# Optimization experiments

Measured on AMD Instinct MI355X. Metric: run time of the kernel, lower is better.

## Reference

```python
import jax, jax.numpy as jnp
import numpy as np

D_MODEL = 1024
N_HEADS = 16
D_K = D_MODEL // N_HEADS
B, S = 8, 1024
EPS = 1e-8


def setup_inputs() -> dict:
    key = jax.random.key(0)
    ks = jax.random.split(key, 6)
    scale = 1.0 / np.sqrt(D_MODEL)
    return {
        "Q_in": jax.random.normal(ks[0], (B, S, D_MODEL), jnp.float32),
        "mask": jax.random.randint(ks[1], (B, 1, S, S), 0, 2, jnp.int32),
        "Wq": jax.random.normal(ks[2], (D_MODEL, D_MODEL), jnp.float32) * scale,
        "bq": jnp.zeros((D_MODEL,), jnp.float32),
        "Wk": jax.random.normal(ks[3], (D_MODEL, D_MODEL), jnp.float32) * scale,
        "bk": jnp.zeros((D_MODEL,), jnp.float32),
        "Wv": jax.random.normal(ks[4], (D_MODEL, D_MODEL), jnp.float32) * scale,
        "bv": jnp.zeros((D_MODEL,), jnp.float32),
        "Wo": jax.random.normal(ks[5], (D_MODEL, D_MODEL), jnp.float32) * scale,
        "bo": jnp.zeros((D_MODEL,), jnp.float32),
    }


def reference(Q_in, mask, Wq, bq, Wk, bk, Wv, bv, Wo, bo):
    # QKV projections: [B,S,D] -> [B,H,S,d_k]
    def split_heads(x):
        return x.reshape(B, S, N_HEADS, D_K).transpose(0, 2, 1, 3)

    Q = split_heads(Q_in @ Wq + bq)
    K = split_heads(Q_in @ Wk + bk)
    V = split_heads(Q_in @ Wv + bv)

    # scaled scores [B,H,S,S], standard softmax
    scores = jnp.einsum("bhqd,bhkd->bhqk", Q, K) / jnp.sqrt(
        jnp.asarray(D_K, jnp.float32))
    scores = jax.nn.softmax(scores, axis=-1)
    # non-standard: multiplicative mask AFTER softmax, then row renorm
    scores = scores * mask.astype(scores.dtype)
    attn = scores / (jnp.sum(scores, axis=-1, keepdims=True) + EPS)

    context = jnp.einsum("bhqk,bhkd->bhqd", attn, V)
    context = context.transpose(0, 2, 1, 3).reshape(B, S, D_MODEL)
    return context @ Wo + bo
```

## Files before the change

### kernel.cpp

```cpp
#include <hip/hip_runtime.h>
#include <hip/hip_bf16.h>
#include <stdint.h>

typedef __attribute__((ext_vector_type(4))) float f32x4;
typedef __attribute__((ext_vector_type(8))) __bf16 bf16x8;
typedef unsigned short u16;
typedef unsigned int u32;
typedef unsigned long long u64;

#define NH 16
#define DKK 64

__device__ __forceinline__ u16 f2bf(float f) {
    u32 u = __builtin_bit_cast(u32, f);
    u32 r = (u + 0x7fffu + ((u >> 16) & 1u)) >> 16;
    return (u16)r;
}

__device__ __forceinline__ u16 cvt_bf(float f) {
    __hip_bfloat16 h = __float2bfloat16(f);
    return *reinterpret_cast<u16*>(&h);
}

__device__ __forceinline__ void gload16(const void* g, void* l) {
    __builtin_amdgcn_global_load_lds((const __attribute__((address_space(1))) void*)g,
                                     (__attribute__((address_space(3))) void*)l, 16, 0, 0);
}

__global__ __launch_bounds__(256) void k_convert_x(const float* __restrict__ x,
                                                   u16* __restrict__ xb) {
    int i = blockIdx.x * 256 + threadIdx.x;
    const float4* p = (const float4*)x + (size_t)i * 2;
    float4 a = p[0], b = p[1];
    union { u16 h[8]; uint4 q; } o;
    o.h[0] = f2bf(a.x); o.h[1] = f2bf(a.y); o.h[2] = f2bf(a.z); o.h[3] = f2bf(a.w);
    o.h[4] = f2bf(b.x); o.h[5] = f2bf(b.y); o.h[6] = f2bf(b.z); o.h[7] = f2bf(b.w);
    ((uint4*)xb)[i] = o.q;
}

__global__ __launch_bounds__(256) void k_convert_w(const float* __restrict__ wq,
                                                   const float* __restrict__ wk,
                                                   const float* __restrict__ wv,
                                                   const float* __restrict__ wo,
                                                   u16* __restrict__ wt) {
    int z = blockIdx.z;
    const float* w = (z == 0) ? wq : (z == 1) ? wk : (z == 2) ? wv : wo;
    __shared__ float t[32][33];
    int tx = threadIdx.x & 31, ty = threadIdx.x >> 5;
    int n0 = blockIdx.x * 32, k0 = blockIdx.y * 32;
    for (int rr = 0; rr < 4; ++rr)
        t[ty + rr * 8][tx] = w[(size_t)(k0 + ty + rr * 8) * 1024 + n0 + tx];
    __syncthreads();
    for (int rr = 0; rr < 4; ++rr) {
        int n = n0 + ty + rr * 8;
        wt[((size_t)z * 1024 + n) * 1024 + k0 + tx] = f2bf(t[tx][ty + rr * 8]);
    }
}

__global__ __launch_bounds__(256) void k_maskpack(const int* __restrict__ mask,
                                                  u64* __restrict__ mb) {
    int wid = (blockIdx.x * 256 + threadIdx.x) >> 6;
    int lane = threadIdx.x & 63;
    for (int c = wid; c < 8 * 1024 * 16; c += 8192) {
        int m = mask[(size_t)c * 64 + lane];
        u64 bits = __ballot(m != 0);
        if (lane == 0)
            mb[(c & 0xFFFFC000u) | ((c & 15) << 10) | ((c >> 4) & 1023)] = bits;
    }
}

template <int MODE>
__global__ __launch_bounds__(256) void k_gemm(const u16* __restrict__ A,
                                              const u16* __restrict__ Bt,
                                              const float* __restrict__ b0,
                                              const float* __restrict__ b1,
                                              const float* __restrict__ b2,
                                              u16* __restrict__ q_out,
                                              u16* __restrict__ k_out,
                                              u16* __restrict__ v_out,
                                              float* __restrict__ out) {
    __shared__ u16 As[128 * 32];
    __shared__ u16 Bs[128 * 32];
    int tid = threadIdx.x;
    int wv = tid >> 6, lane = tid & 63;
    int r = lane & 15, g = lane >> 4;
    int wr = wv >> 1, wc = wv & 1;
    int m0 = blockIdx.x * 128, n0 = blockIdx.y * 128;
    f32x4 acc[4][4] = {};
    for (int kt = 0; kt < 1024; kt += 32) {
        __syncthreads();
        for (int i = 0; i < 2; ++i) {
            int e = i * 256 + tid;
            int row = e >> 2, c8 = (e & 3) * 8;
            const u16* ga = A + (size_t)(m0 + row) * 1024 + kt + c8;
            const u16* gb = Bt + (size_t)(n0 + row) * 1024 + kt + c8;
            gload16(ga, As + (size_t)(i * 256 + wv * 64) * 8);
            gload16(gb, Bs + (size_t)(i * 256 + wv * 64) * 8);
        }
        __syncthreads();
        bf16x8 aF[4], bF[4];
        for (int m = 0; m < 4; ++m) aF[m] = *(const bf16x8*)&As[(wr * 64 + m * 16 + r) * 32 + g * 8];
        for (int n = 0; n < 4; ++n) bF[n] = *(const bf16x8*)&Bs[(wc * 64 + n * 16 + r) * 32 + g * 8];
        for (int m = 0; m < 4; ++m)
            for (int n = 0; n < 4; ++n)
                acc[m][n] = __builtin_amdgcn_mfma_f32_16x16x32_bf16(aF[m], bF[n], acc[m][n], 0, 0, 0);
    }
    for (int m = 0; m < 4; ++m) {
        int rowb = m0 + wr * 64 + m * 16 + 4 * g;
        for (int n = 0; n < 4; ++n) {
            int col = n0 + wc * 64 + n * 16 + r;
            if (MODE == 0) {
                int w = col >> 10, cn = col & 1023;
                const float* bp = (w == 0) ? b0 : (w == 1) ? b1 : b2;
                u16* dst = (w == 0) ? q_out : (w == 1) ? k_out : v_out;
                float sc = (w == 0) ? 0.125f : 1.0f;
                int h = cn >> 6, d = cn & 63;
                float bias = bp[cn];
                for (int i = 0; i < 4; ++i) {
                    int row = rowb + i;
                    int b = row >> 10, s = row & 1023;
                    float v = (acc[m][n][i] + bias) * sc;
                    dst[((size_t)(b * NH + h) * 1024 + s) * 64 + d] = f2bf(v);
                }
            } else {
                float bias = b0[col];
                for (int i = 0; i < 4; ++i) {
                    int row = rowb + i;
                    out[(size_t)row * 1024 + col] = acc[m][n][i] + bias;
                }
            }
        }
    }
}

__global__ __launch_bounds__(256) void k_transpose_v(const u16* __restrict__ vb,
                                                     u16* __restrict__ vt) {
    __shared__ u16 t[64][72];
    int bh = blockIdx.y, s0 = blockIdx.x * 64;
    int tid = threadIdx.x;
    for (int i = 0; i < 2; ++i) {
        int e = i * 256 + tid;
        int row = e >> 3, ch = (e & 7) * 8;
        uint4 v = *(const uint4*)(vb + ((size_t)bh * 1024 + s0 + row) * 64 + ch);
        *(uint4*)&t[row][ch] = v;
    }
    __syncthreads();
    for (int i = 0; i < 2; ++i) {
        int e = i * 256 + tid;
        int d = e >> 3, ch = (e & 7) * 8;
        union { u16 h[8]; uint4 q; } o;
        for (int j = 0; j < 8; ++j) o.h[j] = t[ch + j][d];
        *(uint4*)(vt + ((size_t)bh * 64 + d) * 1024 + s0 + ch) = o.q;
    }
}

__global__ __launch_bounds__(256, 3) void k_attn(const u16* __restrict__ qb,
                                                 const u16* __restrict__ kb,
                                                 const u16* __restrict__ vt,
                                                 const u64* __restrict__ mbits,
                                                 u16* __restrict__ ctx) {
    __shared__ u16 Kd[2][64 * 64];
    __shared__ u16 Vd[2][64 * 64];
    int tid = threadIdx.x, wv = tid >> 6, lane = tid & 63;
    int r = lane & 15, g = lane >> 4;
    int q0 = blockIdx.x * 128, bh = blockIdx.y;
    int b = bh >> 4, h = bh & 15;

    bf16x8 aq[2][2];
    for (int qg = 0; qg < 2; ++qg) {
        const u16* qp = qb + ((size_t)bh * 1024 + q0 + wv * 32 + qg * 16 + r) * 64 + g * 8;
        aq[qg][0] = *(const bf16x8*)qp;
        aq[qg][1] = *(const bf16x8*)(qp + 32);
    }

    f32x4 of[2][4] = {};
    f32x4 zacc[2] = {};
    const bf16x8 vone = {(__bf16)1.f, (__bf16)1.f, (__bf16)1.f, (__bf16)1.f,
                         (__bf16)1.f, (__bf16)1.f, (__bf16)1.f, (__bf16)1.f};

    const u64* mrow = mbits + ((size_t)b * 16) * 1024 + q0 + wv * 32 + r;
    u64 mbc[2] = {mrow[0], mrow[16]};

    for (int i2 = 0; i2 < 2; ++i2) {
        int e = i2 * 256 + tid;
        int s = e >> 3, c = e & 7;
        int cs = (c ^ (s & 7)) * 8;
        int kr = (s & 0x20) | ((s & 0x0C) << 1) | ((s & 0x10) >> 2) | (s & 3);
        gload16(kb + ((size_t)bh * 1024 + kr) * 64 + cs, Kd[0] + (size_t)e * 8);
        gload16(vt + ((size_t)bh * 64 + s) * 1024 + cs, Vd[0] + (size_t)e * 8);
    }
    __syncthreads();

    for (int t = 0; t < 16; ++t) {
        int cur = t & 1;
        u64 mbn0 = 0, mbn1 = 0;
        if (t < 15) {
            int ktn = (t + 1) * 64;
            for (int i2 = 0; i2 < 2; ++i2) {
                int e = i2 * 256 + tid;
                int s = e >> 3, c = e & 7;
                int cs = (c ^ (s & 7)) * 8;
                int kr = (s & 0x20) | ((s & 0x0C) << 1) | ((s & 0x10) >> 2) | (s & 3);
                gload16(kb + ((size_t)bh * 1024 + ktn + kr) * 64 + cs, Kd[cur ^ 1] + (size_t)e * 8);
                gload16(vt + ((size_t)bh * 64 + s) * 1024 + ktn + cs, Vd[cur ^ 1] + (size_t)e * 8);
            }
            mbn0 = mrow[(size_t)(t + 1) * 1024];
            mbn1 = mrow[(size_t)(t + 1) * 1024 + 16];
        }
        const u16* K = Kd[cur];
        const u16* V = Vd[cur];

        bf16x8 bk0[4], bk1[4];
#pragma unroll
        for (int nf = 0; nf < 4; ++nf) {
            int rowk = (nf * 16 + r) * 64;
            bk0[nf] = *(const bf16x8*)&K[rowk + ((g ^ (r & 7)) << 3)];
            bk1[nf] = *(const bf16x8*)&K[rowk + (((g + 4) ^ (r & 7)) << 3)];
        }

        bf16x8 pfr[2][2];
#pragma unroll
        for (int qg = 0; qg < 2; ++qg) {
            f32x4 sf[4];
#pragma unroll
            for (int nf = 0; nf < 4; ++nf) {
                f32x4 z = {0.f, 0.f, 0.f, 0.f};
                z = __builtin_amdgcn_mfma_f32_16x16x32_bf16(bk0[nf], aq[qg][0], z, 0, 0, 0);
                sf[nf] = __builtin_amdgcn_mfma_f32_16x16x32_bf16(bk1[nf], aq[qg][1], z, 0, 0, 0);
            }
            u64 m64 = mbc[qg] >> (g * 8);
            u32 mlo = (u32)m64, mhi = (u32)(m64 >> 32);
            u32 pw[8];
#pragma unroll
            for (int nf = 0; nf < 4; ++nf) {
                u32 nib = ((nf & 2) ? mhi : mlo) >> ((nf & 1) * 4);
                u32 pm0 = ((nib & 1) ? 0xFFFFu : 0u) | ((nib & 2) ? 0xFFFF0000u : 0u);
                u32 pm1 = ((nib & 4) ? 0xFFFFu : 0u) | ((nib & 8) ? 0xFFFF0000u : 0u);
                float e0 = __expf(sf[nf][0]), e1 = __expf(sf[nf][1]);
                float e2 = __expf(sf[nf][2]), e3 = __expf(sf[nf][3]);
                pw[2 * nf]     = (((u32)cvt_bf(e0)) | ((u32)cvt_bf(e1) << 16)) & pm0;
                pw[2 * nf + 1] = (((u32)cvt_bf(e2)) | ((u32)cvt_bf(e3) << 16)) & pm1;
            }
            union { u32 w[4]; bf16x8 v; } f0, f1;
            f0.w[0] = pw[0]; f0.w[1] = pw[1]; f0.w[2] = pw[2]; f0.w[3] = pw[3];
            f1.w[0] = pw[4]; f1.w[1] = pw[5]; f1.w[2] = pw[6]; f1.w[3] = pw[7];
            pfr[qg][0] = f0.v;
            pfr[qg][1] = f1.v;
            zacc[qg] = __builtin_amdgcn_mfma_f32_16x16x32_bf16(vone, pfr[qg][0], zacc[qg], 0, 0, 0);
            zacc[qg] = __builtin_amdgcn_mfma_f32_16x16x32_bf16(vone, pfr[qg][1], zacc[qg], 0, 0, 0);
        }
#pragma unroll
        for (int ks = 0; ks < 2; ++ks) {
#pragma unroll
            for (int nf = 0; nf < 4; ++nf) {
                bf16x8 av = *(const bf16x8*)&V[(nf * 16 + r) * 64 + (((ks * 4 + g) ^ (r & 7)) << 3)];
                of[0][nf] = __builtin_amdgcn_mfma_f32_16x16x32_bf16(av, pfr[0][ks], of[0][nf], 0, 0, 0);
                of[1][nf] = __builtin_amdgcn_mfma_f32_16x16x32_bf16(av, pfr[1][ks], of[1][nf], 0, 0, 0);
            }
        }
        mbc[0] = mbn0;
        mbc[1] = mbn1;
        __syncthreads();
    }

    for (int qg = 0; qg < 2; ++qg) {
        float inv = 1.0f / zacc[qg][0];
        int qrow = q0 + wv * 32 + qg * 16 + r;
        u16* crow = ctx + ((size_t)(b * 1024 + qrow)) * 1024 + h * 64;
#pragma unroll
        for (int nf = 0; nf < 4; ++nf) {
            u32 w0 = ((u32)cvt_bf(of[qg][nf][0] * inv)) | ((u32)cvt_bf(of[qg][nf][1] * inv) << 16);
            u32 w1 = ((u32)cvt_bf(of[qg][nf][2] * inv)) | ((u32)cvt_bf(of[qg][nf][3] * inv) << 16);
            *(u32*)(crow + nf * 16 + g * 4) = w0;
            *(u32*)(crow + nf * 16 + g * 4 + 2) = w1;
        }
    }
}

extern "C" void kernel_launch(void* const* d_in, const int* in_sizes, int n_in,
                              void* d_out, int out_size, void* d_ws, size_t ws_size,
                              hipStream_t stream) {
    const float* Q_in = (const float*)d_in[0];
    const int*   mask = (const int*)d_in[1];
    const float* Wq = (const float*)d_in[2];
    const float* bq = (const float*)d_in[3];
    const float* Wk = (const float*)d_in[4];
    const float* bk = (const float*)d_in[5];
    const float* Wv = (const float*)d_in[6];
    const float* bv = (const float*)d_in[7];
    const float* Wo = (const float*)d_in[8];
    const float* bo = (const float*)d_in[9];

    char* ws = (char*)d_ws;
    u16* Xb = (u16*)(ws);
    u16* Wt = (u16*)(ws + 16777216);
    u16* Qb = (u16*)(ws + 25165824);
    u16* Kb = (u16*)(ws + 41943040);
    u16* Vb = (u16*)(ws + 58720256);
    u16* Vt = (u16*)(ws + 75497472);
    u64* Mb = (u64*)(ws + 92274688);
    u16* Ctx = Vb;

    k_convert_x<<<4096, 256, 0, stream>>>(Q_in, Xb);
    k_convert_w<<<dim3(32, 32, 4), 256, 0, stream>>>(Wq, Wk, Wv, Wo, Wt);
    k_maskpack<<<2048, 256, 0, stream>>>(mask, Mb);
    k_gemm<0><<<dim3(64, 24), 256, 0, stream>>>(Xb, Wt, bq, bk, bv, Qb, Kb, Vb, nullptr);
    k_transpose_v<<<dim3(16, 128), 256, 0, stream>>>(Vb, Vt);
    k_attn<<<dim3(8, 128), 256, 0, stream>>>(Qb, Kb, Vt, Mb, Ctx);
    k_gemm<1><<<dim3(64, 8), 256, 0, stream>>>(Ctx, Wt + (size_t)3 * 1024 * 1024,
                                               bo, nullptr, nullptr,
                                               nullptr, nullptr, nullptr, (float*)d_out);
}
```

Before: 178.4 us.

## Double-buffer GEMM LDS with XOR swizzle and write V transposed in epilogue

The GEMM main loop now double-buffers A/B tiles in shared memory, issuing the next tile's async loads before computing the current one, with one barrier per iteration. LDS columns are XOR-swizzled to cut bank conflicts on fragment reads. The QKV epilogue writes V directly in [bh,d,s] layout as packed 64-bit stores, which removes the separate transpose kernel and its extra round trip through global memory. Shared memory per block doubles, which may lower occupancy.

```diff
diff --git a/kernel.cpp b/kernel.cpp
--- a/kernel.cpp
+++ b/kernel.cpp
@@ -79,48 +79,80 @@
                                               u16* __restrict__ k_out,
                                               u16* __restrict__ v_out,
                                               float* __restrict__ out) {
-    __shared__ u16 As[128 * 32];
-    __shared__ u16 Bs[128 * 32];
+    __shared__ u16 As[2][128 * 32];
+    __shared__ u16 Bs[2][128 * 32];
     int tid = threadIdx.x;
     int wv = tid >> 6, lane = tid & 63;
     int r = lane & 15, g = lane >> 4;
     int wr = wv >> 1, wc = wv & 1;
     int m0 = blockIdx.x * 128, n0 = blockIdx.y * 128;
     f32x4 acc[4][4] = {};
-    for (int kt = 0; kt < 1024; kt += 32) {
-        __syncthreads();
-        for (int i = 0; i < 2; ++i) {
-            int e = i * 256 + tid;
-            int row = e >> 2, c8 = (e & 3) * 8;
-            const u16* ga = A + (size_t)(m0 + row) * 1024 + kt + c8;
-            const u16* gb = Bt + (size_t)(n0 + row) * 1024 + kt + c8;
-            gload16(ga, As + (size_t)(i * 256 + wv * 64) * 8);
-            gload16(gb, Bs + (size_t)(i * 256 + wv * 64) * 8);
-        }
-        __syncthreads();
+
+    int srow0 = tid >> 2, sc0 = ((tid & 3) ^ ((srow0 >> 1) & 3)) * 8;
+    int srow1 = (256 + tid) >> 2, sc1 = ((tid & 3) ^ ((srow1 >> 1) & 3)) * 8;
+    const u16* ga0 = A + (size_t)(m0 + srow0) * 1024 + sc0;
+    const u16* ga1 = A + (size_t)(m0 + srow1) * 1024 + sc1;
+    const u16* gb0 = Bt + (size_t)(n0 + srow0) * 1024 + sc0;
+    const u16* gb1 = Bt + (size_t)(n0 + srow1) * 1024 + sc1;
+
+    gload16(ga0, As[0] + (size_t)tid * 8);
+    gload16(ga1, As[0] + (size_t)(256 + tid) * 8);
+    gload16(gb0, Bs[0] + (size_t)tid * 8);
+    gload16(gb1, Bs[0] + (size_t)(256 + tid) * 8);
+    __syncthreads();
+
+    for (int t = 0; t < 32; ++t) {
+        int cur = t & 1;
+        if (t < 31) {
+            int kt = (t + 1) * 32;
+            gload16(ga0 + kt, As[cur ^ 1] + (size_t)tid * 8);
+            gload16(ga1 + kt, As[cur ^ 1] + (size_t)(256 + tid) * 8);
+            gload16(gb0 + kt, Bs[cur ^ 1] + (size_t)tid * 8);
+            gload16(gb1 + kt, Bs[cur ^ 1] + (size_t)(256 + tid) * 8);
+        }
         bf16x8 aF[4], bF[4];
-        for (int m = 0; m < 4; ++m) aF[m] = *(const bf16x8*)&As[(wr * 64 + m * 16 + r) * 32 + g * 8];
-        for (int n = 0; n < 4; ++n) bF[n] = *(const bf16x8*)&Bs[(wc * 64 + n * 16 + r) * 32 + g * 8];
+#pragma unroll
+        for (int m = 0; m < 4; ++m) {
+            int ro = wr * 64 + m * 16 + r;
+            aF[m] = *(const bf16x8*)&As[cur][ro * 32 + ((g ^ ((ro >> 1) & 3)) << 3)];
+        }
+#pragma unroll
+        for (int n = 0; n < 4; ++n) {
+            int ro = wc * 64 + n * 16 + r;
+            bF[n] = *(const bf16x8*)&Bs[cur][ro * 32 + ((g ^ ((ro >> 1) & 3)) << 3)];
+        }
+#pragma unroll
         for (int m = 0; m < 4; ++m)
+#pragma unroll
             for (int n = 0; n < 4; ++n)
                 acc[m][n] = __builtin_amdgcn_mfma_f32_16x16x32_bf16(aF[m], bF[n], acc[m][n], 0, 0, 0);
-    }
+        __syncthreads();
+    }
+
     for (int m = 0; m < 4; ++m) {
         int rowb = m0 + wr * 64 + m * 16 + 4 * g;
         for (int n = 0; n < 4; ++n) {
             int col = n0 + wc * 64 + n * 16 + r;
             if (MODE == 0) {
                 int w = col >> 10, cn = col & 1023;
-                const float* bp = (w == 0) ? b0 : (w == 1) ? b1 : b2;
-                u16* dst = (w == 0) ? q_out : (w == 1) ? k_out : v_out;
-                float sc = (w == 0) ? 0.125f : 1.0f;
-                int h = cn >> 6, d = cn & 63;
-                float bias = bp[cn];
-                for (int i = 0; i < 4; ++i) {
-                    int row = rowb + i;
-                    int b = row >> 10, s = row & 1023;
-                    float v = (acc[m][n][i] + bias) * sc;
-                    dst[((size_t)(b * NH + h) * 1024 + s) * 64 + d] = f2bf(v);
+                int bb = rowb >> 10, s = rowb & 1023;
+                if (w == 2) {
+                    int h = cn >> 6, d = cn & 63;
+                    float bias = b2[cn];
+                    u64 pk = 0;
+                    for (int i = 0; i < 4; ++i)
+                        pk |= (u64)cvt_bf(acc[m][n][i] + bias) << (16 * i);
+                    *(u64*)(v_out + ((size_t)((bb * NH + h) * 64 + d)) * 1024 + s) = pk;
+                } else {
+                    const float* bp = (w == 0) ? b0 : b1;
+                    u16* dst = (w == 0) ? q_out : k_out;
+                    float sc = (w == 0) ? 0.125f : 1.0f;
+                    int h = cn >> 6, d = cn & 63;
+                    float bias = bp[cn];
+                    for (int i = 0; i < 4; ++i) {
+                        float v = (acc[m][n][i] + bias) * sc;
+                        dst[((size_t)(bb * NH + h) * 1024 + s + i) * 64 + d] = f2bf(v);
+                    }
                 }
             } else {
                 float bias = b0[col];
@@ -130,27 +162,6 @@
                 }
             }
         }
-    }
-}
-
-__global__ __launch_bounds__(256) void k_transpose_v(const u16* __restrict__ vb,
-                                                     u16* __restrict__ vt) {
-    __shared__ u16 t[64][72];
-    int bh = blockIdx.y, s0 = blockIdx.x * 64;
-    int tid = threadIdx.x;
-    for (int i = 0; i < 2; ++i) {
-        int e = i * 256 + tid;
-        int row = e >> 3, ch = (e & 7) * 8;
-        uint4 v = *(const uint4*)(vb + ((size_t)bh * 1024 + s0 + row) * 64 + ch);
-        *(uint4*)&t[row][ch] = v;
-    }
-    __syncthreads();
-    for (int i = 0; i < 2; ++i) {
-        int e = i * 256 + tid;
-        int d = e >> 3, ch = (e & 7) * 8;
-        union { u16 h[8]; uint4 q; } o;
-        for (int j = 0; j < 8; ++j) o.h[j] = t[ch + j][d];
-        *(uint4*)(vt + ((size_t)bh * 64 + d) * 1024 + s0 + ch) = o.q;
     }
 }
 
@@ -296,16 +307,14 @@
     u16* Wt = (u16*)(ws + 16777216);
     u16* Qb = (u16*)(ws + 25165824);
     u16* Kb = (u16*)(ws + 41943040);
-    u16* Vb = (u16*)(ws + 58720256);
+    u16* Ctx = (u16*)(ws + 58720256);
     u16* Vt = (u16*)(ws + 75497472);
     u64* Mb = (u64*)(ws + 92274688);
-    u16* Ctx = Vb;
 
     k_convert_x<<<4096, 256, 0, stream>>>(Q_in, Xb);
     k_convert_w<<<dim3(32, 32, 4), 256, 0, stream>>>(Wq, Wk, Wv, Wo, Wt);
     k_maskpack<<<2048, 256, 0, stream>>>(mask, Mb);
-    k_gemm<0><<<dim3(64, 24), 256, 0, stream>>>(Xb, Wt, bq, bk, bv, Qb, Kb, Vb, nullptr);
-    k_transpose_v<<<dim3(16, 128), 256, 0, stream>>>(Vb, Vt);
+    k_gemm<0><<<dim3(64, 24), 256, 0, stream>>>(Xb, Wt, bq, bk, bv, Qb, Kb, Vt, nullptr);
     k_attn<<<dim3(8, 128), 256, 0, stream>>>(Qb, Kb, Vt, Mb, Ctx);
     k_gemm<1><<<dim3(64, 8), 256, 0, stream>>>(Ctx, Wt + (size_t)3 * 1024 * 1024,
                                                bo, nullptr, nullptr,
```

Result: slower. 191.3 us (+7.3%).
